# Optimization experiments

Measured on AMD Instinct MI355X. Metric: run time of the kernel, lower is better.

The kernel has to match this reference:

```python
import jax, jax.numpy as jnp
from jax import lax
import numpy as np

DIM = 1024
SEQ = 2048
BATCH = 2
DEPTH = 2
D_INNER = 2 * DIM          # expand=2
D_STATE = 16
D_CONV = 4
DT_RANK = DIM // 16        # ceil(dim/16) = 64
FF = 4 * DIM               # ff_mult=4
EPS = 1e-5


def rmsnorm(x, w, eps=EPS):
    return x * lax.rsqrt(jnp.mean(x * x, axis=-1, keepdims=True) + eps) * w


def layernorm(x, w, b, eps=EPS):
    mu = jnp.mean(x, axis=-1, keepdims=True)
    var = jnp.mean((x - mu) ** 2, axis=-1, keepdims=True)
    return (x - mu) * lax.rsqrt(var + eps) * w + b


def silu(x):
    return x * jax.nn.sigmoid(x)


def causal_conv1d(x, w, b):
    # x: [b, l, d], depthwise causal conv, kernel w: [d, k], bias b: [d]
    xc = jnp.transpose(x, (0, 2, 1))  # [b, d, l]
    y = lax.conv_general_dilated(
        xc, w[:, None, :], window_strides=(1,), padding=[(D_CONV - 1, 0)],
        dimension_numbers=("NCH", "OIH", "NCH"), feature_group_count=D_INNER)
    y = y + b[None, :, None]
    return jnp.transpose(y, (0, 2, 1))  # [b, l, d]


def selective_scan(u, delta, A, B, C, D):
    # u, delta: [b, l, d]; A: [d, n]; B, C: [b, l, n]; D: [d]
    def step(h, inp):
        d_t, b_t, c_t, u_t = inp                       # [b,d],[b,n],[b,n],[b,d]
        dA = jnp.exp(d_t[..., None] * A)               # [b, d, n]
        h = dA * h + (d_t * u_t)[..., None] * b_t[:, None, :]
        y = jnp.einsum("bdn,bn->bd", h, c_t)
        return h, y

    h0 = jnp.zeros((u.shape[0], A.shape[0], A.shape[1]), u.dtype)
    xs = (jnp.swapaxes(delta, 0, 1), jnp.swapaxes(B, 0, 1),
          jnp.swapaxes(C, 0, 1), jnp.swapaxes(u, 0, 1))
    _, ys = lax.scan(step, h0, xs)                     # ys: [l, b, d]
    return jnp.swapaxes(ys, 0, 1) + u * D


def mamba_mixer(h, in_w, cw, cb, xp_w, dtp_w, dtp_b, A_log, D, out_w):
    # h: [b, l, dim]
    xz = jnp.einsum("bld,ed->ble", h, in_w)            # [b, l, 2*d_inner]
    x_in, z = jnp.split(xz, 2, axis=-1)
    x_c = silu(causal_conv1d(x_in, cw, cb))            # [b, l, d_inner]
    x_dbl = jnp.einsum("ble,re->blr", x_c, xp_w)       # [b, l, dt_rank+2n]
    dt = x_dbl[..., :DT_RANK]
    B = x_dbl[..., DT_RANK:DT_RANK + D_STATE]
    C = x_dbl[..., DT_RANK + D_STATE:]
    delta = jax.nn.softplus(jnp.einsum("blr,er->ble", dt, dtp_w) + dtp_b)
    A = -jnp.exp(A_log)
    y = selective_scan(x_c, delta, A, B, C, D)
    y = y * silu(z)
    return jnp.einsum("ble,de->bld", y, out_w)         # [b, l, dim]


def setup_inputs() -> dict:
    key = jax.random.key(0)
    ks = jax.random.split(key, 16)

    def nrm(k, shape, s=0.02):
        return jax.random.normal(k, shape, dtype=jnp.float32) * s

    A_init = jnp.log(jnp.tile(jnp.arange(1, D_STATE + 1, dtype=jnp.float32),
                              (DEPTH, D_INNER, 1)))
    return {
        "x": jax.random.normal(ks[0], (BATCH, SEQ, DIM), jnp.float32),
        "in_proj_w": nrm(ks[1], (DEPTH, 2 * D_INNER, DIM)),
        "conv_w": nrm(ks[2], (DEPTH, D_INNER, D_CONV), 0.1),
        "conv_b": jnp.zeros((DEPTH, D_INNER), jnp.float32),
        "x_proj_w": nrm(ks[3], (DEPTH, DT_RANK + 2 * D_STATE, D_INNER)),
        "dt_proj_w": nrm(ks[4], (DEPTH, D_INNER, DT_RANK), 0.1),
        "dt_proj_b": nrm(ks[5], (DEPTH, D_INNER), 0.1),
        "A_log": A_init,
        "D": jnp.ones((DEPTH, D_INNER), jnp.float32),
        "out_proj_w": nrm(ks[6], (DEPTH, DIM, D_INNER)),
        "rms_w": jnp.ones((DEPTH, DIM), jnp.float32),
        "ln_w": jnp.ones((DEPTH, DIM), jnp.float32),
        "ln_b": jnp.zeros((DEPTH, DIM), jnp.float32),
        "ff_w1": nrm(ks[7], (2 * FF, DIM)),
        "ff_b1": jnp.zeros((2 * FF,), jnp.float32),
        "ff_w2": nrm(ks[8], (DIM, FF)),
        "ff_b2": jnp.zeros((DIM,), jnp.float32),
    }


def reference(x, in_proj_w, conv_w, conv_b, x_proj_w, dt_proj_w, dt_proj_b,
              A_log, D, out_proj_w, rms_w, ln_w, ln_b, ff_w1, ff_b1, ff_w2, ff_b2):
    residual = None
    h = x
    for i in range(in_proj_w.shape[0]):
        # fused add + RMSNorm (prenorm, residual in fp32)
        residual = h if residual is None else residual + h
        normed = rmsnorm(residual, rms_w[i])
        h = mamba_mixer(normed, in_proj_w[i], conv_w[i], conv_b[i],
                        x_proj_w[i], dt_proj_w[i], dt_proj_b[i],
                        A_log[i], D[i], out_proj_w[i])
        # extra per-block LayerNorm on mixer output
        h = layernorm(h, ln_w[i], ln_b[i])
    # final GEGLU feedforward
    u = jnp.einsum("bld,ed->ble", h, ff_w1) + ff_b1    # [b, l, 2*FF]
    a, g = jnp.split(u, 2, axis=-1)
    v = a * jax.nn.gelu(g, approximate=False)
    return jnp.einsum("blf,df->bld", v, ff_w2) + ff_b2
```

## Files before the change

### kernel.cpp

```cpp
#include <hip/hip_runtime.h>
#include <cstdint>
#include <cstddef>

#define DIM     1024
#define SEQ     2048
#define BATCH   2
#define DEPTH   2
#define D_INNER 2048
#define D_STATE 16
#define D_CONV  4
#define DT_RANK 64
#define FF      4096
#define ROWS    (BATCH*SEQ)
#define EPS     1e-5f

#define CS      32
#define NC      (SEQ/CS)
#define NC_LOG  6

#define XP_KS    8
#define XP_KSTEP (D_INNER/XP_KS)

#define LOG2E 1.44269504088896f

typedef unsigned short ushort_t;
typedef short bf16x8 __attribute__((ext_vector_type(8)));
typedef float f32x4  __attribute__((ext_vector_type(4)));

__device__ __forceinline__ float sigmoidf_(float x) { return 1.f / (1.f + __expf(-x)); }

__device__ __forceinline__ ushort_t f2bf(float x) {
  unsigned int u = __float_as_uint(x);
  u += 0x7fffu + ((u >> 16) & 1u);
  return (ushort_t)(u >> 16);
}
__device__ __forceinline__ float bf2f(ushort_t u) {
  return __uint_as_float((unsigned)u << 16);
}

__device__ __forceinline__ void async_cp16(const void* g, void* lds) {
  __builtin_amdgcn_global_load_lds(
      (const __attribute__((address_space(1))) unsigned int*)g,
      (__attribute__((address_space(3))) unsigned int*)lds, 16, 0, 0);
}

__device__ __forceinline__ float2 block_sum2(float a, float b) {
#pragma unroll
  for (int off = 32; off > 0; off >>= 1) {
    a += __shfl_down(a, off, 64);
    b += __shfl_down(b, off, 64);
  }
  __shared__ float sa[4], sb[4];
  __syncthreads();
  if ((threadIdx.x & 63) == 0) { int w = threadIdx.x >> 6; sa[w] = a; sb[w] = b; }
  __syncthreads();
  return make_float2(sa[0] + sa[1] + sa[2] + sa[3], sb[0] + sb[1] + sb[2] + sb[3]);
}

__global__ __launch_bounds__(256) void res_rms_kernel(
    const float* __restrict__ xin, const float* __restrict__ hadd,
    float* __restrict__ res, ushort_t* __restrict__ nrm, const float* __restrict__ w) {
  int row = blockIdx.x;
  const float* xr = xin + (size_t)row * DIM;
  const float* hr = hadd ? hadd + (size_t)row * DIM : nullptr;
  float* rr = res + (size_t)row * DIM;
  ushort_t* nr = nrm + (size_t)row * DIM;
  float v[4]; float ss = 0.f;
#pragma unroll
  for (int i = 0; i < 4; ++i) {
    int j = threadIdx.x + i * 256;
    float t = xr[j];
    if (hr) t += hr[j];
    v[i] = t; rr[j] = t; ss += t * t;
  }
  float2 s = block_sum2(ss, 0.f);
  float rstd = rsqrtf(s.x * (1.f / DIM) + EPS);
#pragma unroll
  for (int i = 0; i < 4; ++i) {
    int j = threadIdx.x + i * 256;
    nr[j] = f2bf(v[i] * rstd * w[j]);
  }
}

__global__ __launch_bounds__(256) void layernorm_kernel(
    const float* __restrict__ in, float* __restrict__ out, ushort_t* __restrict__ outb,
    const float* __restrict__ w, const float* __restrict__ b) {
  int row = blockIdx.x;
  const float* xr = in + (size_t)row * DIM;
  float* orow = out + (size_t)row * DIM;
  ushort_t* obrow = outb + (size_t)row * DIM;
  float v[4]; float s1 = 0.f, s2 = 0.f;
#pragma unroll
  for (int i = 0; i < 4; ++i) {
    int j = threadIdx.x + i * 256;
    float t = xr[j];
    v[i] = t; s1 += t; s2 += t * t;
  }
  float2 s = block_sum2(s1, s2);
  float mean = s.x * (1.f / DIM);
  float var = s.y * (1.f / DIM) - mean * mean;
  float rstd = rsqrtf(var + EPS);
#pragma unroll
  for (int i = 0; i < 4; ++i) {
    int j = threadIdx.x + i * 256;
    float o = (v[i] - mean) * rstd * w[j] + b[j];
    orow[j] = o;
    obrow[j] = f2bf(o);
  }
}

__global__ __launch_bounds__(256) void f2b_kernel(
    const float* __restrict__ s, ushort_t* __restrict__ d, int n) {
  int i = (blockIdx.x * 256 + threadIdx.x) * 4;
  if (i >= n) return;
  float4 v = *reinterpret_cast<const float4*>(s + i);
  d[i + 0] = f2bf(v.x); d[i + 1] = f2bf(v.y);
  d[i + 2] = f2bf(v.z); d[i + 3] = f2bf(v.w);
}

__global__ __launch_bounds__(256) void gemm_bf16_nt(
    const ushort_t* __restrict__ A,
    const ushort_t* __restrict__ B,
    float* __restrict__ C,
    ushort_t* __restrict__ Cb,
    int N, int K,
    const float* __restrict__ bias, int grp) {
  __shared__ ushort_t As[128 * 64];
  __shared__ ushort_t Bs[128 * 64];
  const int tid = threadIdx.x;
  const int l = tid & 63;
  const int w = tid >> 6;

  const unsigned nwgx = gridDim.x;
  const unsigned nwg = nwgx * gridDim.y;
  const unsigned bid = blockIdx.y * nwgx + blockIdx.x;
  const unsigned cpx = nwg >> 3;
  const unsigned s = (bid & 7u) * cpx + (bid >> 3);
  const unsigned bandw = (unsigned)grp * nwgx;
  const unsigned band = s / bandw;
  const unsigned rem = s % bandw;
  const int m0 = (int)(band * grp + (rem % grp)) * 128;
  const int n0 = (int)(rem / grp) * 128;

  const int wm = (w >> 1) * 64;
  const int wn = (w & 1) * 64;

  const int srow = l >> 3;
  const int ksrc = 8 * ((l & 7) ^ srow);
  const int kg = l >> 4;
  const int lr = l & 15;

  f32x4 acc[4][4];
#pragma unroll
  for (int mi = 0; mi < 4; ++mi)
#pragma unroll
    for (int ni = 0; ni < 4; ++ni) acc[mi][ni] = (f32x4)0.f;

  for (int k0 = 0; k0 < K; k0 += 64) {
#pragma unroll
    for (int j = 0; j < 4; ++j) {
      int c = j * 4 + w;
      int r = c * 8 + srow;
      async_cp16(&A[(size_t)(m0 + r) * K + k0 + ksrc], &As[c * 512]);
    }
#pragma unroll
    for (int j = 0; j < 4; ++j) {
      int c = j * 4 + w;
      int r = c * 8 + srow;
      async_cp16(&B[(size_t)(n0 + r) * K + k0 + ksrc], &Bs[c * 512]);
    }
    __syncthreads();
#pragma unroll
    for (int ks = 0; ks < 2; ++ks) {
      bf16x8 af[4], bfr[4];
#pragma unroll
      for (int mi = 0; mi < 4; ++mi) {
        int r = wm + mi * 16 + lr;
        int boff = r * 128 + ((ks * 64 + kg * 16) ^ ((r & 7) << 4));
        af[mi] = *reinterpret_cast<const bf16x8*>(reinterpret_cast<const char*>(As) + boff);
      }
#pragma unroll
      for (int ni = 0; ni < 4; ++ni) {
        int r = wn + ni * 16 + lr;
        int boff = r * 128 + ((ks * 64 + kg * 16) ^ ((r & 7) << 4));
        bfr[ni] = *reinterpret_cast<const bf16x8*>(reinterpret_cast<const char*>(Bs) + boff);
      }
#pragma unroll
      for (int mi = 0; mi < 4; ++mi)
#pragma unroll
        for (int ni = 0; ni < 4; ++ni)
          acc[mi][ni] = __builtin_amdgcn_mfma_f32_16x16x32_bf16(af[mi], bfr[ni], acc[mi][ni], 0, 0, 0);
    }
    __syncthreads();
  }

  const int crow0 = (l >> 4) * 4;
  const int ccol = l & 15;
#pragma unroll
  for (int mi = 0; mi < 4; ++mi) {
#pragma unroll
    for (int ni = 0; ni < 4; ++ni) {
      int col = n0 + wn + ni * 16 + ccol;
      float bv = bias ? bias[col] : 0.f;
#pragma unroll
      for (int j = 0; j < 4; ++j) {
        int row = m0 + wm + mi * 16 + crow0 + j;
        float v = acc[mi][ni][j] + bv;
        if (Cb) Cb[(size_t)row * N + col] = f2bf(v);
        else    C[(size_t)row * N + col] = v;
      }
    }
  }
}

__global__ __launch_bounds__(256) void gemm_bf16_nt64(
    const ushort_t* __restrict__ A,
    const ushort_t* __restrict__ B,
    float* __restrict__ C,
    int N, int K,
    const float* __restrict__ bias, int grp) {
  __shared__ ushort_t As[64 * 64];
  __shared__ ushort_t Bs[128 * 64];
  const int tid = threadIdx.x;
  const int l = tid & 63;
  const int w = tid >> 6;

  const unsigned nwgx = gridDim.x;
  const unsigned nwg = nwgx * gridDim.y;
  const unsigned bid = blockIdx.y * nwgx + blockIdx.x;
  const unsigned cpx = nwg >> 3;
  const unsigned s = (bid & 7u) * cpx + (bid >> 3);
  const unsigned bandw = (unsigned)grp * nwgx;
  const unsigned band = s / bandw;
  const unsigned rem = s % bandw;
  const int m0 = (int)(band * grp + (rem % grp)) * 64;
  const int n0 = (int)(rem / grp) * 128;

  const int wm = (w >> 1) * 32;
  const int wn = (w & 1) * 64;

  const int srow = l >> 3;
  const int ksrc = 8 * ((l & 7) ^ srow);
  const int kg = l >> 4;
  const int lr = l & 15;

  f32x4 acc[2][4];
#pragma unroll
  for (int mi = 0; mi < 2; ++mi)
#pragma unroll
    for (int ni = 0; ni < 4; ++ni) acc[mi][ni] = (f32x4)0.f;

  for (int k0 = 0; k0 < K; k0 += 64) {
#pragma unroll
    for (int j = 0; j < 2; ++j) {
      int c = j * 4 + w;
      int r = c * 8 + srow;
      async_cp16(&A[(size_t)(m0 + r) * K + k0 + ksrc], &As[c * 512]);
    }
#pragma unroll
    for (int j = 0; j < 4; ++j) {
      int c = j * 4 + w;
      int r = c * 8 + srow;
      async_cp16(&B[(size_t)(n0 + r) * K + k0 + ksrc], &Bs[c * 512]);
    }
    __syncthreads();
#pragma unroll
    for (int ks = 0; ks < 2; ++ks) {
      bf16x8 af[2], bfr[4];
#pragma unroll
      for (int mi = 0; mi < 2; ++mi) {
        int r = wm + mi * 16 + lr;
        int boff = r * 128 + ((ks * 64 + kg * 16) ^ ((r & 7) << 4));
        af[mi] = *reinterpret_cast<const bf16x8*>(reinterpret_cast<const char*>(As) + boff);
      }
#pragma unroll
      for (int ni = 0; ni < 4; ++ni) {
        int r = wn + ni * 16 + lr;
        int boff = r * 128 + ((ks * 64 + kg * 16) ^ ((r & 7) << 4));
        bfr[ni] = *reinterpret_cast<const bf16x8*>(reinterpret_cast<const char*>(Bs) + boff);
      }
#pragma unroll
      for (int mi = 0; mi < 2; ++mi)
#pragma unroll
        for (int ni = 0; ni < 4; ++ni)
          acc[mi][ni] = __builtin_amdgcn_mfma_f32_16x16x32_bf16(af[mi], bfr[ni], acc[mi][ni], 0, 0, 0);
    }
    __syncthreads();
  }

  const int crow0 = (l >> 4) * 4;
  const int ccol = l & 15;
#pragma unroll
  for (int mi = 0; mi < 2; ++mi) {
#pragma unroll
    for (int ni = 0; ni < 4; ++ni) {
      int col = n0 + wn + ni * 16 + ccol;
      float bv = bias ? bias[col] : 0.f;
#pragma unroll
      for (int j = 0; j < 4; ++j) {
        int row = m0 + wm + mi * 16 + crow0 + j;
        C[(size_t)row * N + col] = acc[mi][ni][j] + bv;
      }
    }
  }
}

__global__ __launch_bounds__(256) void gemm_ffn1_glu(
    const ushort_t* __restrict__ A,
    const ushort_t* __restrict__ B,
    ushort_t* __restrict__ O,
    int K,
    const float* __restrict__ bias, int grp) {
  __shared__ ushort_t As[128 * 64];
  __shared__ ushort_t Bs[128 * 64];
  const int tid = threadIdx.x;
  const int l = tid & 63;
  const int w = tid >> 6;

  const unsigned nwgx = gridDim.x;
  const unsigned nwg = nwgx * gridDim.y;
  const unsigned bid = blockIdx.y * nwgx + blockIdx.x;
  const unsigned cpx = nwg >> 3;
  const unsigned s = (bid & 7u) * cpx + (bid >> 3);
  const unsigned bandw = (unsigned)grp * nwgx;
  const unsigned band = s / bandw;
  const unsigned rem = s % bandw;
  const int m0 = (int)(band * grp + (rem % grp)) * 128;
  const int n0 = (int)(rem / grp) * 64;

  const int wm = (w >> 1) * 64;
  const int wn2 = (w & 1) * 32;

  const int srow = l >> 3;
  const int ksrc = 8 * ((l & 7) ^ srow);
  const int kg = l >> 4;
  const int lr = l & 15;

  f32x4 acc[4][4];
#pragma unroll
  for (int mi = 0; mi < 4; ++mi)
#pragma unroll
    for (int ni = 0; ni < 4; ++ni) acc[mi][ni] = (f32x4)0.f;

  for (int k0 = 0; k0 < K; k0 += 64) {
#pragma unroll
    for (int j = 0; j < 4; ++j) {
      int c = j * 4 + w;
      int r = c * 8 + srow;
      async_cp16(&A[(size_t)(m0 + r) * K + k0 + ksrc], &As[c * 512]);
    }
#pragma unroll
    for (int j = 0; j < 4; ++j) {
      int c = j * 4 + w;
      int gr = (c < 8) ? (n0 + c * 8 + srow)
                       : (FF + n0 + (c - 8) * 8 + srow);
      async_cp16(&B[(size_t)gr * K + k0 + ksrc], &Bs[c * 512]);
    }
    __syncthreads();
#pragma unroll
    for (int ks = 0; ks < 2; ++ks) {
      bf16x8 af[4], bfr[4];
#pragma unroll
      for (int mi = 0; mi < 4; ++mi) {
        int r = wm + mi * 16 + lr;
        int boff = r * 128 + ((ks * 64 + kg * 16) ^ ((r & 7) << 4));
        af[mi] = *reinterpret_cast<const bf16x8*>(reinterpret_cast<const char*>(As) + boff);
      }
#pragma unroll
      for (int ni = 0; ni < 4; ++ni) {
        int r = (ni < 2 ? wn2 + ni * 16 : 64 + wn2 + (ni - 2) * 16) + lr;
        int boff = r * 128 + ((ks * 64 + kg * 16) ^ ((r & 7) << 4));
        bfr[ni] = *reinterpret_cast<const bf16x8*>(reinterpret_cast<const char*>(Bs) + boff);
      }
#pragma unroll
      for (int mi = 0; mi < 4; ++mi)
#pragma unroll
        for (int ni = 0; ni < 4; ++ni)
          acc[mi][ni] = __builtin_amdgcn_mfma_f32_16x16x32_bf16(af[mi], bfr[ni], acc[mi][ni], 0, 0, 0);
    }
    __syncthreads();
  }

  const int crow0 = (l >> 4) * 4;
  const int ccol = l & 15;
#pragma unroll
  for (int mi = 0; mi < 4; ++mi) {
#pragma unroll
    for (int ni = 0; ni < 2; ++ni) {
      int col = n0 + wn2 + ni * 16 + ccol;
      float ba = bias[col];
      float bg = bias[FF + col];
#pragma unroll
      for (int j = 0; j < 4; ++j) {
        int row = m0 + wm + mi * 16 + crow0 + j;
        float a = acc[mi][ni][j] + ba;
        float g = acc[mi][ni + 2][j] + bg;
        float ge = 0.5f * g * (1.f + erff(g * 0.70710678118654752f));
        O[(size_t)row * FF + col] = f2bf(a * ge);
      }
    }
  }
}

__global__ __launch_bounds__(256) void gemm_nt(
    const float* __restrict__ A, int lda,
    const float* __restrict__ B, int ldb,
    float* __restrict__ C, int ldc,
    int N, int K,
    const float* __restrict__ bias, int act) {
  __shared__ __align__(16) float Asf[16][68];
  __shared__ __align__(16) float Bsf[16][68];
  const int tx = threadIdx.x;
  const int ty = threadIdx.y;
  const int tid = ty * 16 + tx;
  const int m0 = blockIdx.y * 64;
  const int n0 = blockIdx.x * 64;
  const int lrow = tid >> 2;
  const int lk = (tid & 3) * 4;

  float acc[4][4] = {{0.f}};

  for (int k0 = 0; k0 < K; k0 += 16) {
    float4 av, bv;
    {
      const float* ap = A + (size_t)(m0 + lrow) * lda + k0 + lk;
      av = *reinterpret_cast<const float4*>(ap);
    }
    int brow = n0 + lrow;
    if (brow < N) {
      const float* bp = B + (size_t)brow * ldb + k0 + lk;
      bv = *reinterpret_cast<const float4*>(bp);
    } else {
      bv = make_float4(0.f, 0.f, 0.f, 0.f);
    }
    __syncthreads();
    Asf[lk + 0][lrow] = av.x; Asf[lk + 1][lrow] = av.y;
    Asf[lk + 2][lrow] = av.z; Asf[lk + 3][lrow] = av.w;
    Bsf[lk + 0][lrow] = bv.x; Bsf[lk + 1][lrow] = bv.y;
    Bsf[lk + 2][lrow] = bv.z; Bsf[lk + 3][lrow] = bv.w;
    __syncthreads();
#pragma unroll
    for (int k = 0; k < 16; ++k) {
      const float4 a4 = *reinterpret_cast<const float4*>(&Asf[k][ty * 4]);
      const float4 b4 = *reinterpret_cast<const float4*>(&Bsf[k][tx * 4]);
      float a[4] = {a4.x, a4.y, a4.z, a4.w};
      float bb[4] = {b4.x, b4.y, b4.z, b4.w};
#pragma unroll
      for (int i = 0; i < 4; ++i)
#pragma unroll
        for (int j = 0; j < 4; ++j)
          acc[i][j] = fmaf(a[i], bb[j], acc[i][j]);
    }
  }

#pragma unroll
  for (int i = 0; i < 4; ++i) {
    int m = m0 + ty * 4 + i;
#pragma unroll
    for (int j = 0; j < 4; ++j) {
      int n = n0 + tx * 4 + j;
      if (n < N) {
        float v = acc[i][j];
        if (bias) v += bias[n];
        if (act == 1) v = (v > 20.f) ? v : log1pf(__expf(v));
        C[(size_t)m * ldc + n] = v;
      }
    }
  }
}

__global__ __launch_bounds__(256) void xproj_partial(
    const float* __restrict__ A,
    const float* __restrict__ W,
    float* __restrict__ pbuf) {
  __shared__ __align__(16) float As[64][68];
  __shared__ __align__(16) float Wsd[96][68];
  const int ks = blockIdx.x;
  const int mb = blockIdx.y;
  const int tid = threadIdx.x;
  const int r0 = (tid >> 4) * 4;
  const int c0 = (tid & 15) * 6;

  float acc[4][6];
#pragma unroll
  for (int i = 0; i < 4; ++i)
#pragma unroll
    for (int j = 0; j < 6; ++j) acc[i][j] = 0.f;

  for (int k0 = 0; k0 < XP_KSTEP; k0 += 64) {
    const int kbase = ks * XP_KSTEP + k0;
    __syncthreads();
    {
      int r = tid >> 2, c = (tid & 3) * 16;
      const float* src = A + (size_t)(mb * 64 + r) * D_INNER + kbase + c;
#pragma unroll
      for (int q = 0; q < 4; ++q)
        *reinterpret_cast<float4*>(&As[r][c + q * 4]) =
            *reinterpret_cast<const float4*>(src + q * 4);
    }
#pragma unroll
    for (int q = 0; q < 6; ++q) {
      int f = q * 256 + tid;
      int wr = f >> 4;
      int wc = (f & 15) * 4;
      *reinterpret_cast<float4*>(&Wsd[wr][wc]) =
          *reinterpret_cast<const float4*>(&W[(size_t)wr * D_INNER + kbase + wc]);
    }
    __syncthreads();
#pragma unroll 16
    for (int k = 0; k < 64; ++k) {
      float a[4], wv[6];
#pragma unroll
      for (int i = 0; i < 4; ++i) a[i] = As[r0 + i][k];
#pragma unroll
      for (int j = 0; j < 6; ++j) wv[j] = Wsd[c0 + j][k];
#pragma unroll
      for (int i = 0; i < 4; ++i)
#pragma unroll
        for (int j = 0; j < 6; ++j)
          acc[i][j] = fmaf(a[i], wv[j], acc[i][j]);
    }
  }

  float* dst = pbuf + ((size_t)ks * ROWS + mb * 64) * 96;
#pragma unroll
  for (int i = 0; i < 4; ++i)
#pragma unroll
    for (int j = 0; j < 6; ++j)
      dst[(size_t)(r0 + i) * 96 + c0 + j] = acc[i][j];
}

__global__ __launch_bounds__(256) void xproj_reduce(
    const float* __restrict__ pbuf, float* __restrict__ xdbl) {
  int i = blockIdx.x * 256 + threadIdx.x;
  float s = 0.f;
#pragma unroll
  for (int ks = 0; ks < XP_KS; ++ks)
    s += pbuf[(size_t)ks * (ROWS * 96) + i];
  xdbl[i] = s;
}

__global__ __launch_bounds__(256) void conv_silu_kernel(
    const ushort_t* __restrict__ xzb, float* __restrict__ xc,
    const float* __restrict__ cw, const float* __restrict__ cb) {
  int t = (blockIdx.x * 256 + threadIdx.x) * 4;
  if (t >= ROWS * D_INNER) return;
  int d = t & (D_INNER - 1);
  int row = t >> 11;
  int l = row & (SEQ - 1);
  float acc[4];
#pragma unroll
  for (int q = 0; q < 4; ++q) acc[q] = cb[d + q];
#pragma unroll
  for (int j = 0; j < 4; ++j) {
    int ls = l - 3 + j;
    if (ls >= 0) {
      ushort4 uv = *reinterpret_cast<const ushort4*>(
          xzb + (size_t)(row - 3 + j) * (2 * D_INNER) + d);
      acc[0] = fmaf(cw[(d + 0) * 4 + j], bf2f(uv.x), acc[0]);
      acc[1] = fmaf(cw[(d + 1) * 4 + j], bf2f(uv.y), acc[1]);
      acc[2] = fmaf(cw[(d + 2) * 4 + j], bf2f(uv.z), acc[2]);
      acc[3] = fmaf(cw[(d + 3) * 4 + j], bf2f(uv.w), acc[3]);
    }
  }
  float4 o;
  o.x = acc[0] * sigmoidf_(acc[0]);
  o.y = acc[1] * sigmoidf_(acc[1]);
  o.z = acc[2] * sigmoidf_(acc[2]);
  o.w = acc[3] * sigmoidf_(acc[3]);
  *reinterpret_cast<float4*>(xc + t) = o;
}

__global__ __launch_bounds__(256) void scan_pass1(
    const float* __restrict__ delta,
    const float* __restrict__ xc,
    const float* __restrict__ xdbl,
    const float* __restrict__ A_log,
    float* __restrict__ harr,
    float* __restrict__ dtsum) {
  __shared__ __align__(16) float Bls[CS][16];
  int gid = blockIdx.x * 256 + threadIdx.x;
  int d = gid & (D_INNER - 1);
  int bc = gid >> 11;
  int c = bc & (NC - 1);
  int b = bc >> NC_LOG;
  const size_t r0 = (size_t)b * SEQ + (size_t)c * CS;

  if (threadIdx.x < CS * 4) {
    int sl = threadIdx.x >> 2, sf = (threadIdx.x & 3) * 4;
    *reinterpret_cast<f32x4*>(&Bls[sl][sf]) =
        *reinterpret_cast<const f32x4*>(xdbl + (r0 + sl) * 96 + 64 + sf);
  }

  float Av2[D_STATE];
#pragma unroll
  for (int n = 0; n < D_STATE; ++n)
    Av2[n] = -__expf(A_log[(size_t)d * D_STATE + n]) * LOG2E;
  float h[D_STATE];
#pragma unroll
  for (int n = 0; n < D_STATE; ++n) h[n] = 0.f;
  float dts = 0.f;

  const float* drow = delta + r0 * D_INNER + d;
  const float* urow = xc + r0 * D_INNER + d;

  float pdt[4], pu[4];
#pragma unroll
  for (int g = 0; g < 4; ++g) {
    pdt[g] = drow[(size_t)g * D_INNER];
    pu[g]  = urow[(size_t)g * D_INNER];
  }
  __syncthreads();

  for (int l0 = 0; l0 < CS; l0 += 4) {
    float cdt[4], cu[4];
#pragma unroll
    for (int g = 0; g < 4; ++g) { cdt[g] = pdt[g]; cu[g] = pu[g]; }
    if (l0 + 4 < CS) {
#pragma unroll
      for (int g = 0; g < 4; ++g) {
        pdt[g] = drow[(size_t)(l0 + 4 + g) * D_INNER];
        pu[g]  = urow[(size_t)(l0 + 4 + g) * D_INNER];
      }
    }
#pragma unroll
    for (int g = 0; g < 4; ++g) {
      int l = l0 + g;
      f32x4 B0 = *reinterpret_cast<const f32x4*>(&Bls[l][0]);
      f32x4 B1 = *reinterpret_cast<const f32x4*>(&Bls[l][4]);
      f32x4 B2 = *reinterpret_cast<const f32x4*>(&Bls[l][8]);
      f32x4 B3 = *reinterpret_cast<const f32x4*>(&Bls[l][12]);
      float du = cdt[g] * cu[g];
      dts += cdt[g];
      float Bsr[D_STATE] = {B0[0],B0[1],B0[2],B0[3], B1[0],B1[1],B1[2],B1[3],
                            B2[0],B2[1],B2[2],B2[3], B3[0],B3[1],B3[2],B3[3]};
#pragma unroll
      for (int n = 0; n < D_STATE; ++n) {
        float dA = __builtin_amdgcn_exp2f(cdt[g] * Av2[n]);
        h[n] = dA * h[n] + du * Bsr[n];
      }
    }
  }
#pragma unroll
  for (int n = 0; n < D_STATE; ++n)
    harr[((size_t)bc * D_STATE + n) * D_INNER + d] = h[n];
  dtsum[(size_t)bc * D_INNER + d] = dts;
}

__global__ __launch_bounds__(256) void scan_pass2(
    float* __restrict__ harr,
    const float* __restrict__ dtsum,
    const float* __restrict__ A_log) {
  int gid = blockIdx.x * 256 + threadIdx.x;
  int d = gid & (D_INNER - 1);
  int bn = gid >> 11;
  int n = bn & (D_STATE - 1);
  int b = bn >> 4;
  float Av2 = -__expf(A_log[(size_t)d * D_STATE + n]) * LOG2E;
  float h = 0.f;
  for (int c = 0; c < NC; ++c) {
    size_t bc = (size_t)b * NC + c;
    size_t idx = (bc * D_STATE + n) * D_INNER + d;
    float he = harr[idx];
    harr[idx] = h;
    float P = __builtin_amdgcn_exp2f(Av2 * dtsum[bc * D_INNER + d]);
    h = P * h + he;
  }
}

__global__ __launch_bounds__(256) void scan_pass3(
    const float* __restrict__ delta,
    const float* __restrict__ xc,
    ushort_t* __restrict__ ybf,
    const float* __restrict__ xdbl,
    const ushort_t* __restrict__ xzb,
    const float* __restrict__ A_log,
    const float* __restrict__ Dp,
    const float* __restrict__ harr) {
  __shared__ __align__(16) float BCls[CS][32];
  int gid = blockIdx.x * 256 + threadIdx.x;
  int d = gid & (D_INNER - 1);
  int bc = gid >> 11;
  int c = bc & (NC - 1);
  int b = bc >> NC_LOG;
  const size_t r0 = (size_t)b * SEQ + (size_t)c * CS;

  {
    int sl = threadIdx.x >> 3, sf = (threadIdx.x & 7) * 4;
    *reinterpret_cast<f32x4*>(&BCls[sl][sf]) =
        *reinterpret_cast<const f32x4*>(xdbl + (r0 + sl) * 96 + 64 + sf);
  }

  float Av2[D_STATE];
#pragma unroll
  for (int n = 0; n < D_STATE; ++n)
    Av2[n] = -__expf(A_log[(size_t)d * D_STATE + n]) * LOG2E;
  const float Dd = Dp[d];
  float h[D_STATE];
#pragma unroll
  for (int n = 0; n < D_STATE; ++n)
    h[n] = harr[((size_t)bc * D_STATE + n) * D_INNER + d];

  const float* drow = delta + r0 * D_INNER + d;
  const float* urow = xc + r0 * D_INNER + d;
  const ushort_t* zrow = xzb + r0 * (2 * D_INNER) + D_INNER + d;
  ushort_t* yrow = ybf + r0 * D_INNER + d;

  float pdt[4], pu[4], pz[4];
#pragma unroll
  for (int g = 0; g < 4; ++g) {
    pdt[g] = drow[(size_t)g * D_INNER];
    pu[g]  = urow[(size_t)g * D_INNER];
    pz[g]  = bf2f(zrow[(size_t)g * (2 * D_INNER)]);
  }
  __syncthreads();

  for (int l0 = 0; l0 < CS; l0 += 4) {
    float cdt[4], cu[4], cz[4];
#pragma unroll
    for (int g = 0; g < 4; ++g) { cdt[g] = pdt[g]; cu[g] = pu[g]; cz[g] = pz[g]; }
    if (l0 + 4 < CS) {
#pragma unroll
      for (int g = 0; g < 4; ++g) {
        pdt[g] = drow[(size_t)(l0 + 4 + g) * D_INNER];
        pu[g]  = urow[(size_t)(l0 + 4 + g) * D_INNER];
        pz[g]  = bf2f(zrow[(size_t)(l0 + 4 + g) * (2 * D_INNER)]);
      }
    }
#pragma unroll
    for (int g = 0; g < 4; ++g) {
      int l = l0 + g;
      f32x4 B0 = *reinterpret_cast<const f32x4*>(&BCls[l][0]);
      f32x4 B1 = *reinterpret_cast<const f32x4*>(&BCls[l][4]);
      f32x4 B2 = *reinterpret_cast<const f32x4*>(&BCls[l][8]);
      f32x4 B3 = *reinterpret_cast<const f32x4*>(&BCls[l][12]);
      f32x4 C0 = *reinterpret_cast<const f32x4*>(&BCls[l][16]);
      f32x4 C1 = *reinterpret_cast<const f32x4*>(&BCls[l][20]);
      f32x4 C2 = *reinterpret_cast<const f32x4*>(&BCls[l][24]);
      f32x4 C3 = *reinterpret_cast<const f32x4*>(&BCls[l][28]);
      float du = cdt[g] * cu[g];
      float Bsr[D_STATE] = {B0[0],B0[1],B0[2],B0[3], B1[0],B1[1],B1[2],B1[3],
                            B2[0],B2[1],B2[2],B2[3], B3[0],B3[1],B3[2],B3[3]};
      float Csr[D_STATE] = {C0[0],C0[1],C0[2],C0[3], C1[0],C1[1],C1[2],C1[3],
                            C2[0],C2[1],C2[2],C2[3], C3[0],C3[1],C3[2],C3[3]};
      float y = 0.f;
#pragma unroll
      for (int n = 0; n < D_STATE; ++n) {
        float dA = __builtin_amdgcn_exp2f(cdt[g] * Av2[n]);
        h[n] = dA * h[n] + du * Bsr[n];
        y = fmaf(h[n], Csr[n], y);
      }
      y = fmaf(cu[g], Dd, y);
      yrow[(size_t)l * D_INNER] = f2bf(y * (cz[g] * sigmoidf_(cz[g])));
    }
  }
}

extern "C" void kernel_launch(void* const* d_in, const int* in_sizes, int n_in,
                              void* d_out, int out_size, void* d_ws, size_t ws_size,
                              hipStream_t stream) {
  const float* x         = (const float*)d_in[0];
  const float* in_proj_w = (const float*)d_in[1];
  const float* conv_w    = (const float*)d_in[2];
  const float* conv_b    = (const float*)d_in[3];
  const float* x_proj_w  = (const float*)d_in[4];
  const float* dt_proj_w = (const float*)d_in[5];
  const float* dt_proj_b = (const float*)d_in[6];
  const float* A_log     = (const float*)d_in[7];
  const float* Dp        = (const float*)d_in[8];
  const float* out_proj_w= (const float*)d_in[9];
  const float* rms_w     = (const float*)d_in[10];
  const float* ln_w      = (const float*)d_in[11];
  const float* ln_b      = (const float*)d_in[12];
  const float* ff_w1     = (const float*)d_in[13];
  const float* ff_b1     = (const float*)d_in[14];
  const float* ff_w2     = (const float*)d_in[15];
  const float* ff_b2     = (const float*)d_in[16];
  float* out = (float*)d_out;

  float* ws = (float*)d_ws;
  float* res     = ws;
  float* hbuf    = ws + 4194304;
  float* xdbl    = ws + 8388608;
  float* dtsum   = ws + 4194304;
  ushort_t* hbuf_bf = (ushort_t*)(ws + 8912896);
  float*    pbuf    = ws + 11010048;
  ushort_t* y_bf    = (ushort_t*)(ws + 15204352);
  ushort_t* glu_bf  = (ushort_t*)(ws + 11010048);
  float* big   = ws + 19398656;
  ushort_t* xz_bf = (ushort_t*)big;
  float* xc    = big + 8388608;
  float* delta = big + 16777216;
  float* harr  = big + 25165824;
  float* op_out= big;
  ushort_t* nrm_bf = (ushort_t*)delta;
  ushort_t* in_w_bf  = (ushort_t*)(ws + 52953088);
  ushort_t* out_w_bf = (ushort_t*)(ws + 57147392);
  ushort_t* ff1_bf   = (ushort_t*)(ws + 59244544);
  ushort_t* ff2_bf   = (ushort_t*)(ws + 63438848);

  dim3 tb(16, 16);

  f2b_kernel<<<8192, 256, 0, stream>>>(in_proj_w, in_w_bf, 8388608);
  f2b_kernel<<<4096, 256, 0, stream>>>(out_proj_w, out_w_bf, 4194304);
  f2b_kernel<<<8192, 256, 0, stream>>>(ff_w1, ff1_bf, 8388608);
  f2b_kernel<<<4096, 256, 0, stream>>>(ff_w2, ff2_bf, 4194304);

  for (int i = 0; i < DEPTH; ++i) {
    const float* cw    = conv_w + (size_t)i * D_INNER * D_CONV;
    const float* cb    = conv_b + (size_t)i * D_INNER;
    const float* xp_w  = x_proj_w + (size_t)i * 96 * D_INNER;
    const float* dtp_w = dt_proj_w + (size_t)i * D_INNER * DT_RANK;
    const float* dtp_b = dt_proj_b + (size_t)i * D_INNER;
    const float* Alg   = A_log + (size_t)i * D_INNER * D_STATE;
    const float* Di    = Dp + (size_t)i * D_INNER;

    res_rms_kernel<<<ROWS, 256, 0, stream>>>(i == 0 ? x : res, i == 0 ? nullptr : hbuf,
                                             res, nrm_bf, rms_w + (size_t)i * DIM);
    gemm_bf16_nt<<<dim3(32, 32), 256, 0, stream>>>(
        nrm_bf, in_w_bf + (size_t)i * 4194304, nullptr, xz_bf, 2 * D_INNER, DIM,
        nullptr, 16);
    conv_silu_kernel<<<(ROWS * D_INNER / 4) / 256, 256, 0, stream>>>(xz_bf, xc, cw, cb);
    xproj_partial<<<dim3(XP_KS, 64), 256, 0, stream>>>(xc, xp_w, pbuf);
    xproj_reduce<<<(ROWS * 96) / 256, 256, 0, stream>>>(pbuf, xdbl);
    gemm_nt<<<dim3(32, 64), tb, 0, stream>>>(xdbl, 96, dtp_w, DT_RANK, delta, D_INNER,
                                             D_INNER, DT_RANK, dtp_b, 1);
    scan_pass1<<<(BATCH * NC * D_INNER) / 256, 256, 0, stream>>>(delta, xc, xdbl, Alg,
                                                                 harr, dtsum);
    scan_pass2<<<(BATCH * D_STATE * D_INNER) / 256, 256, 0, stream>>>(harr, dtsum, Alg);
    scan_pass3<<<(BATCH * NC * D_INNER) / 256, 256, 0, stream>>>(delta, xc, y_bf, xdbl,
                                                                 xz_bf, Alg, Di, harr);
    gemm_bf16_nt64<<<dim3(8, 64), 256, 0, stream>>>(
        y_bf, out_w_bf + (size_t)i * 2097152, op_out, DIM, D_INNER, nullptr, 8);
    layernorm_kernel<<<ROWS, 256, 0, stream>>>(op_out, hbuf, hbuf_bf,
                                               ln_w + (size_t)i * DIM, ln_b + (size_t)i * DIM);
  }

  gemm_ffn1_glu<<<dim3(64, 32), 256, 0, stream>>>(hbuf_bf, ff1_bf, glu_bf, DIM,
                                                  ff_b1, 16);
  gemm_bf16_nt64<<<dim3(8, 64), 256, 0, stream>>>(glu_bf, ff2_bf, out, DIM, FF,
                                                  ff_b2, 8);
}
```

Measured before the change: 790.6 us.

## Fuse LayerNorm with residual RMSNorm, store conv output as bf16, merge weight casts

Fuses each block's output LayerNorm with the next block's residual add and RMSNorm, so the fp32 normalized output no longer makes a round trip through memory and one launch per layer goes away. The conv+SiLU activation is now stored as bf16 rather than fp32, which halves the traffic for the x-projection and both scan passes. The four weight-cast launches are merged into one kernel. Rounding the activation that feeds the scan and the x-projection to bf16 adds precision loss.

```diff
diff --git a/kernel.cpp b/kernel.cpp
--- a/kernel.cpp
+++ b/kernel.cpp
@@ -58,11 +58,10 @@
 }
 
 __global__ __launch_bounds__(256) void res_rms_kernel(
-    const float* __restrict__ xin, const float* __restrict__ hadd,
+    const float* __restrict__ xin,
     float* __restrict__ res, ushort_t* __restrict__ nrm, const float* __restrict__ w) {
   int row = blockIdx.x;
   const float* xr = xin + (size_t)row * DIM;
-  const float* hr = hadd ? hadd + (size_t)row * DIM : nullptr;
   float* rr = res + (size_t)row * DIM;
   ushort_t* nr = nrm + (size_t)row * DIM;
   float v[4]; float ss = 0.f;
@@ -70,7 +69,6 @@
   for (int i = 0; i < 4; ++i) {
     int j = threadIdx.x + i * 256;
     float t = xr[j];
-    if (hr) t += hr[j];
     v[i] = t; rr[j] = t; ss += t * t;
   }
   float2 s = block_sum2(ss, 0.f);
@@ -82,13 +80,14 @@
   }
 }
 
-__global__ __launch_bounds__(256) void layernorm_kernel(
-    const float* __restrict__ in, float* __restrict__ out, ushort_t* __restrict__ outb,
-    const float* __restrict__ w, const float* __restrict__ b) {
+__global__ __launch_bounds__(256) void ln_res_rms_kernel(
+    const float* __restrict__ in, float* __restrict__ res,
+    const float* __restrict__ lw, const float* __restrict__ lb,
+    const float* __restrict__ rw, ushort_t* __restrict__ nrm) {
   int row = blockIdx.x;
   const float* xr = in + (size_t)row * DIM;
-  float* orow = out + (size_t)row * DIM;
-  ushort_t* obrow = outb + (size_t)row * DIM;
+  float* rr = res + (size_t)row * DIM;
+  ushort_t* nr = nrm + (size_t)row * DIM;
   float v[4]; float s1 = 0.f, s2 = 0.f;
 #pragma unroll
   for (int i = 0; i < 4; ++i) {
@@ -100,22 +99,62 @@
   float mean = s.x * (1.f / DIM);
   float var = s.y * (1.f / DIM) - mean * mean;
   float rstd = rsqrtf(var + EPS);
+  float t4[4]; float ss = 0.f;
 #pragma unroll
   for (int i = 0; i < 4; ++i) {
     int j = threadIdx.x + i * 256;
-    float o = (v[i] - mean) * rstd * w[j] + b[j];
-    orow[j] = o;
-    obrow[j] = f2bf(o);
-  }
-}
-
-__global__ __launch_bounds__(256) void f2b_kernel(
-    const float* __restrict__ s, ushort_t* __restrict__ d, int n) {
+    float o = (v[i] - mean) * rstd * lw[j] + lb[j];
+    float t = rr[j] + o;
+    rr[j] = t;
+    t4[i] = t; ss += t * t;
+  }
+  float2 s2v = block_sum2(ss, 0.f);
+  float rstd2 = rsqrtf(s2v.x * (1.f / DIM) + EPS);
+#pragma unroll
+  for (int i = 0; i < 4; ++i) {
+    int j = threadIdx.x + i * 256;
+    nr[j] = f2bf(t4[i] * rstd2 * rw[j]);
+  }
+}
+
+__global__ __launch_bounds__(256) void ln_final_kernel(
+    const float* __restrict__ in, ushort_t* __restrict__ outb,
+    const float* __restrict__ w, const float* __restrict__ b) {
+  int row = blockIdx.x;
+  const float* xr = in + (size_t)row * DIM;
+  ushort_t* obrow = outb + (size_t)row * DIM;
+  float v[4]; float s1 = 0.f, s2 = 0.f;
+#pragma unroll
+  for (int i = 0; i < 4; ++i) {
+    int j = threadIdx.x + i * 256;
+    float t = xr[j];
+    v[i] = t; s1 += t; s2 += t * t;
+  }
+  float2 s = block_sum2(s1, s2);
+  float mean = s.x * (1.f / DIM);
+  float var = s.y * (1.f / DIM) - mean * mean;
+  float rstd = rsqrtf(var + EPS);
+#pragma unroll
+  for (int i = 0; i < 4; ++i) {
+    int j = threadIdx.x + i * 256;
+    obrow[j] = f2bf((v[i] - mean) * rstd * w[j] + b[j]);
+  }
+}
+
+__global__ __launch_bounds__(256) void f2b_all(
+    const float* __restrict__ w0, ushort_t* __restrict__ d0,
+    const float* __restrict__ w1, ushort_t* __restrict__ d1,
+    const float* __restrict__ w2, ushort_t* __restrict__ d2,
+    const float* __restrict__ w3, ushort_t* __restrict__ d3) {
   int i = (blockIdx.x * 256 + threadIdx.x) * 4;
-  if (i >= n) return;
-  float4 v = *reinterpret_cast<const float4*>(s + i);
-  d[i + 0] = f2bf(v.x); d[i + 1] = f2bf(v.y);
-  d[i + 2] = f2bf(v.z); d[i + 3] = f2bf(v.w);
+  const float* s; ushort_t* d; int off;
+  if (i < 8388608)        { s = w0; d = d0; off = i; }
+  else if (i < 12582912)  { s = w1; d = d1; off = i - 8388608; }
+  else if (i < 20971520)  { s = w2; d = d2; off = i - 12582912; }
+  else                    { s = w3; d = d3; off = i - 20971520; }
+  float4 v = *reinterpret_cast<const float4*>(s + off);
+  d[off + 0] = f2bf(v.x); d[off + 1] = f2bf(v.y);
+  d[off + 2] = f2bf(v.z); d[off + 3] = f2bf(v.w);
 }
 
 __global__ __launch_bounds__(256) void gemm_bf16_nt(
@@ -470,7 +509,7 @@
 }
 
 __global__ __launch_bounds__(256) void xproj_partial(
-    const float* __restrict__ A,
+    const ushort_t* __restrict__ A,
     const float* __restrict__ W,
     float* __restrict__ pbuf) {
   __shared__ __align__(16) float As[64][68];
@@ -492,11 +531,15 @@
     __syncthreads();
     {
       int r = tid >> 2, c = (tid & 3) * 16;
-      const float* src = A + (size_t)(mb * 64 + r) * D_INNER + kbase + c;
-#pragma unroll
-      for (int q = 0; q < 4; ++q)
-        *reinterpret_cast<float4*>(&As[r][c + q * 4]) =
-            *reinterpret_cast<const float4*>(src + q * 4);
+      const ushort_t* src = A + (size_t)(mb * 64 + r) * D_INNER + kbase + c;
+#pragma unroll
+      for (int q = 0; q < 4; ++q) {
+        ushort4 uv = *reinterpret_cast<const ushort4*>(src + q * 4);
+        As[r][c + q * 4 + 0] = bf2f(uv.x);
+        As[r][c + q * 4 + 1] = bf2f(uv.y);
+        As[r][c + q * 4 + 2] = bf2f(uv.z);
+        As[r][c + q * 4 + 3] = bf2f(uv.w);
+      }
     }
 #pragma unroll
     for (int q = 0; q < 6; ++q) {
@@ -541,7 +584,7 @@
 }
 
 __global__ __launch_bounds__(256) void conv_silu_kernel(
-    const ushort_t* __restrict__ xzb, float* __restrict__ xc,
+    const ushort_t* __restrict__ xzb, ushort_t* __restrict__ xcb,
     const float* __restrict__ cw, const float* __restrict__ cb) {
   int t = (blockIdx.x * 256 + threadIdx.x) * 4;
   if (t >= ROWS * D_INNER) return;
@@ -563,17 +606,17 @@
       acc[3] = fmaf(cw[(d + 3) * 4 + j], bf2f(uv.w), acc[3]);
     }
   }
-  float4 o;
-  o.x = acc[0] * sigmoidf_(acc[0]);
-  o.y = acc[1] * sigmoidf_(acc[1]);
-  o.z = acc[2] * sigmoidf_(acc[2]);
-  o.w = acc[3] * sigmoidf_(acc[3]);
-  *reinterpret_cast<float4*>(xc + t) = o;
+  ushort4 o;
+  o.x = f2bf(acc[0] * sigmoidf_(acc[0]));
+  o.y = f2bf(acc[1] * sigmoidf_(acc[1]));
+  o.z = f2bf(acc[2] * sigmoidf_(acc[2]));
+  o.w = f2bf(acc[3] * sigmoidf_(acc[3]));
+  *reinterpret_cast<ushort4*>(xcb + t) = o;
 }
 
 __global__ __launch_bounds__(256) void scan_pass1(
     const float* __restrict__ delta,
-    const float* __restrict__ xc,
+    const ushort_t* __restrict__ xcb,
     const float* __restrict__ xdbl,
     const float* __restrict__ A_log,
     float* __restrict__ harr,
@@ -602,13 +645,13 @@
   float dts = 0.f;
 
   const float* drow = delta + r0 * D_INNER + d;
-  const float* urow = xc + r0 * D_INNER + d;
+  const ushort_t* urow = xcb + r0 * D_INNER + d;
 
   float pdt[4], pu[4];
 #pragma unroll
   for (int g = 0; g < 4; ++g) {
     pdt[g] = drow[(size_t)g * D_INNER];
-    pu[g]  = urow[(size_t)g * D_INNER];
+    pu[g]  = bf2f(urow[(size_t)g * D_INNER]);
   }
   __syncthreads();
 
@@ -620,7 +663,7 @@
 #pragma unroll
       for (int g = 0; g < 4; ++g) {
         pdt[g] = drow[(size_t)(l0 + 4 + g) * D_INNER];
-        pu[g]  = urow[(size_t)(l0 + 4 + g) * D_INNER];
+        pu[g]  = bf2f(urow[(size_t)(l0 + 4 + g) * D_INNER]);
       }
     }
 #pragma unroll
@@ -670,7 +713,7 @@
 
 __global__ __launch_bounds__(256) void scan_pass3(
     const float* __restrict__ delta,
-    const float* __restrict__ xc,
+    const ushort_t* __restrict__ xcb,
     ushort_t* __restrict__ ybf,
     const float* __restrict__ xdbl,
     const ushort_t* __restrict__ xzb,
@@ -702,7 +745,7 @@
     h[n] = harr[((size_t)bc * D_STATE + n) * D_INNER + d];
 
   const float* drow = delta + r0 * D_INNER + d;
-  const float* urow = xc + r0 * D_INNER + d;
+  const ushort_t* urow = xcb + r0 * D_INNER + d;
   const ushort_t* zrow = xzb + r0 * (2 * D_INNER) + D_INNER + d;
   ushort_t* yrow = ybf + r0 * D_INNER + d;
 
@@ -710,7 +753,7 @@
 #pragma unroll
   for (int g = 0; g < 4; ++g) {
     pdt[g] = drow[(size_t)g * D_INNER];
-    pu[g]  = urow[(size_t)g * D_INNER];
+    pu[g]  = bf2f(urow[(size_t)g * D_INNER]);
     pz[g]  = bf2f(zrow[(size_t)g * (2 * D_INNER)]);
   }
   __syncthreads();
@@ -723,7 +766,7 @@
 #pragma unroll
       for (int g = 0; g < 4; ++g) {
         pdt[g] = drow[(size_t)(l0 + 4 + g) * D_INNER];
-        pu[g]  = urow[(size_t)(l0 + 4 + g) * D_INNER];
+        pu[g]  = bf2f(urow[(size_t)(l0 + 4 + g) * D_INNER]);
         pz[g]  = bf2f(zrow[(size_t)(l0 + 4 + g) * (2 * D_INNER)]);
       }
     }
@@ -780,16 +823,15 @@
 
   float* ws = (float*)d_ws;
   float* res     = ws;
-  float* hbuf    = ws + 4194304;
+  float* dtsum   = ws + 4194304;
   float* xdbl    = ws + 8388608;
-  float* dtsum   = ws + 4194304;
   ushort_t* hbuf_bf = (ushort_t*)(ws + 8912896);
   float*    pbuf    = ws + 11010048;
   ushort_t* y_bf    = (ushort_t*)(ws + 15204352);
   ushort_t* glu_bf  = (ushort_t*)(ws + 11010048);
   float* big   = ws + 19398656;
   ushort_t* xz_bf = (ushort_t*)big;
-  float* xc    = big + 8388608;
+  ushort_t* xcb   = (ushort_t*)(big + 8388608);
   float* delta = big + 16777216;
   float* harr  = big + 25165824;
   float* op_out= big;
@@ -801,10 +843,10 @@
 
   dim3 tb(16, 16);
 
-  f2b_kernel<<<8192, 256, 0, stream>>>(in_proj_w, in_w_bf, 8388608);
-  f2b_kernel<<<4096, 256, 0, stream>>>(out_proj_w, out_w_bf, 4194304);
-  f2b_kernel<<<8192, 256, 0, stream>>>(ff_w1, ff1_bf, 8388608);
-  f2b_kernel<<<4096, 256, 0, stream>>>(ff_w2, ff2_bf, 4194304);
+  f2b_all<<<24576, 256, 0, stream>>>(in_proj_w, in_w_bf, out_proj_w, out_w_bf,
+                                     ff_w1, ff1_bf, ff_w2, ff2_bf);
+
+  res_rms_kernel<<<ROWS, 256, 0, stream>>>(x, res, nrm_bf, rms_w);
 
   for (int i = 0; i < DEPTH; ++i) {
     const float* cw    = conv_w + (size_t)i * D_INNER * D_CONV;
@@ -815,25 +857,29 @@
     const float* Alg   = A_log + (size_t)i * D_INNER * D_STATE;
     const float* Di    = Dp + (size_t)i * D_INNER;
 
-    res_rms_kernel<<<ROWS, 256, 0, stream>>>(i == 0 ? x : res, i == 0 ? nullptr : hbuf,
-                                             res, nrm_bf, rms_w + (size_t)i * DIM);
     gemm_bf16_nt<<<dim3(32, 32), 256, 0, stream>>>(
         nrm_bf, in_w_bf + (size_t)i * 4194304, nullptr, xz_bf, 2 * D_INNER, DIM,
         nullptr, 16);
-    conv_silu_kernel<<<(ROWS * D_INNER / 4) / 256, 256, 0, stream>>>(xz_bf, xc, cw, cb);
-    xproj_partial<<<dim3(XP_KS, 64), 256, 0, stream>>>(xc, xp_w, pbuf);
+    conv_silu_kernel<<<(ROWS * D_INNER / 4) / 256, 256, 0, stream>>>(xz_bf, xcb, cw, cb);
+    xproj_partial<<<dim3(XP_KS, 64), 256, 0, stream>>>(xcb, xp_w, pbuf);
     xproj_reduce<<<(ROWS * 96) / 256, 256, 0, stream>>>(pbuf, xdbl);
     gemm_nt<<<dim3(32, 64), tb, 0, stream>>>(xdbl, 96, dtp_w, DT_RANK, delta, D_INNER,
                                              D_INNER, DT_RANK, dtp_b, 1);
-    scan_pass1<<<(BATCH * NC * D_INNER) / 256, 256, 0, stream>>>(delta, xc, xdbl, Alg,
+    scan_pass1<<<(BATCH * NC * D_INNER) / 256, 256, 0, stream>>>(delta, xcb, xdbl, Alg,
                                                                  harr, dtsum);
     scan_pass2<<<(BATCH * D_STATE * D_INNER) / 256, 256, 0, stream>>>(harr, dtsum, Alg);
-    scan_pass3<<<(BATCH * NC * D_INNER) / 256, 256, 0, stream>>>(delta, xc, y_bf, xdbl,
+    scan_pass3<<<(BATCH * NC * D_INNER) / 256, 256, 0, stream>>>(delta, xcb, y_bf, xdbl,
                                                                  xz_bf, Alg, Di, harr);
     gemm_bf16_nt64<<<dim3(8, 64), 256, 0, stream>>>(
         y_bf, out_w_bf + (size_t)i * 2097152, op_out, DIM, D_INNER, nullptr, 8);
-    layernorm_kernel<<<ROWS, 256, 0, stream>>>(op_out, hbuf, hbuf_bf,
-                                               ln_w + (size_t)i * DIM, ln_b + (size_t)i * DIM);
+    if (i + 1 < DEPTH) {
+      ln_res_rms_kernel<<<ROWS, 256, 0, stream>>>(
+          op_out, res, ln_w + (size_t)i * DIM, ln_b + (size_t)i * DIM,
+          rms_w + (size_t)(i + 1) * DIM, nrm_bf);
+    } else {
+      ln_final_kernel<<<ROWS, 256, 0, stream>>>(
+          op_out, hbuf_bf, ln_w + (size_t)i * DIM, ln_b + (size_t)i * DIM);
+    }
   }
 
   gemm_ffn1_glu<<<dim3(64, 32), 256, 0, stream>>>(hbuf_bf, ff1_bf, glu_bf, DIM,
```

After: 759.9 us. 1.04x faster.
